# Kernel optimization log

Hardware: AMD Instinct MI355X
Metric: run time of the kernel (lower is better)

Reference implementation:

```python
import jax, jax.numpy as jnp
import numpy as np

N, E = 40000, 640000
D, H, DK = 128, 8, 16   # out_dim, n_heads, d_k = D // H
T, R = 3, 4             # num node types, num relation types


def setup_inputs() -> dict:
    key = jax.random.key(0)
    ks = jax.random.split(key, 16)
    glorot = lambda k, shape, fan: jax.random.normal(k, shape, jnp.float32) * np.sqrt(2.0 / fan)
    inp = {
        'node_inp': jax.random.normal(ks[0], (N, D), jnp.float32),
        'node_type': jax.random.randint(ks[1], (N,), 0, T),
        'edge_index': jax.random.randint(ks[2], (2, E), 0, N),
        'edge_type': jax.random.randint(ks[3], (E,), 0, R),
        'node_position': jax.random.randint(ks[4], (N,), 0, N),
        # per-node-type Linear weights, stored [T, in, out] (y = x @ W + b)
        'Kw': glorot(ks[5], (T, D, D), 2 * D), 'Kb': jnp.zeros((T, D), jnp.float32),
        'Qw': glorot(ks[6], (T, D, D), 2 * D), 'Qb': jnp.zeros((T, D), jnp.float32),
        'Vw': glorot(ks[7], (T, D, D), 2 * D), 'Vb': jnp.zeros((T, D), jnp.float32),
        'Aw': glorot(ks[8], (T, D, D), 2 * D), 'Ab': jnp.zeros((T, D), jnp.float32),
        'relation_pri': jnp.ones((T, R, T, H), jnp.float32),
        'relation_att': glorot(ks[9], (R, H, DK, DK), 2 * DK),
        'relation_msg': glorot(ks[10], (R, H, DK, DK), 2 * DK),
        'relation_s2u': glorot(ks[11], (D, D), 2 * D),
        'skip': jnp.ones((T,), jnp.float32),
    }
    return inp


def reference(node_inp, node_type, edge_index, edge_type, node_position,
              Kw, Kb, Qw, Qb, Vw, Vb, Aw, Ab,
              relation_pri, relation_att, relation_msg, relation_s2u, skip):
    n = node_inp.shape[0]
    src, tgt = edge_index[0], edge_index[1]  # j (source), i (target)
    ar = jnp.arange(n)

    # per-type K/Q/V projections for every node: [T, N, D], then select own type
    k_all = jnp.einsum('nd,tdo->tno', node_inp, Kw) + Kb[:, None, :]
    q_all = jnp.einsum('nd,tdo->tno', node_inp, Qw) + Qb[:, None, :]
    v_all = jnp.einsum('nd,tdo->tno', node_inp, Vw) + Vb[:, None, :]
    k_node = k_all[node_type, ar]
    q_node = q_all[node_type, ar]
    v_node = v_all[node_type, ar]

    k_j = k_node[src].reshape(-1, H, DK)
    v_j = v_node[src].reshape(-1, H, DK)
    q_i = q_node[tgt].reshape(-1, H, DK)

    # per-relation attention / message transforms (select per edge relation)
    k_t = jnp.zeros_like(k_j)
    v_t = jnp.zeros_like(v_j)
    for r in range(R):
        sel = (edge_type == r)[:, None, None]
        k_t = jnp.where(sel, jnp.einsum('ehd,hdf->ehf', k_j, relation_att[r]), k_t)
        v_t = jnp.where(sel, jnp.einsum('ehd,hdf->ehf', v_j, relation_msg[r]), v_t)

    st, tt = node_type[src], node_type[tgt]
    pri = relation_pri[tt, edge_type, st]                       # [E, H]
    att_raw = (q_i * k_t).sum(-1) * pri / np.sqrt(DK)           # [E, H]

    # scatter-softmax over edges sharing the same target node
    m = jax.ops.segment_max(att_raw, tgt, num_segments=n)
    m = jnp.where(jnp.isfinite(m), m, 0.0)
    ex = jnp.exp(att_raw - m[tgt])
    den = jax.ops.segment_sum(ex, tgt, num_segments=n)
    att = ex / (den[tgt] + 1e-16)

    msg = (v_t * att[:, :, None]).reshape(-1, D)
    aggr = jax.ops.segment_sum(msg, tgt, num_segments=n)        # scatter-add

    # speaker information: edges with edge_type==0, message from target rep to source index
    sp_in = v_all[1][tgt]                                       # v_linears[1](node_inp[edge_index_i])
    sp_msg = sp_in @ relation_s2u                               # [E, D]
    drop_idx = jnp.where(edge_type == 0, src, n)                # out-of-range -> dropped
    speaker_info = jnp.zeros((n, D), node_inp.dtype).at[drop_idx].set(sp_msg, mode='drop')

    aggr = jax.nn.gelu(aggr + speaker_info, approximate=False)

    # target-specific aggregation with per-type learnable skip (dropout=eval identity)
    a_all = jnp.einsum('no,tof->tnf', aggr, Aw) + Ab[:, None, :]
    a_node = a_all[node_type, ar]
    alpha = jax.nn.sigmoid(skip)[node_type][:, None]
    return a_node * alpha + node_inp * (1.0 - alpha)
```

## Files before the change

kernel.cpp:

```cpp
#include <hip/hip_runtime.h>
#include <hip/hip_bf16.h>
#include <math.h>

#define ND 128
#define NH 8
#define DKK 16
#define NT 3
#define NR 4
#define NB 8
#define NMAT 12
#define SCB 4096

typedef unsigned short ushort_t;
typedef __bf16 bf16_t;
typedef bf16_t bf16x8 __attribute__((ext_vector_type(8)));
typedef float f32x4 __attribute__((ext_vector_type(4)));

__device__ __forceinline__ float bf2f(unsigned short u) {
    union { unsigned int i; float f; } v; v.i = ((unsigned int)u) << 16; return v.f;
}
__device__ __forceinline__ unsigned short f2bf(float f) {
    union { float f; unsigned int i; } v; v.f = f;
    unsigned int x = v.i;
    unsigned int lsb = (x >> 16) & 1u;
    x += 0x7fffu + lsb;
    return (unsigned short)(x >> 16);
}
__device__ __forceinline__ unsigned int pk2(float a, float b) {
    return (unsigned int)f2bf(a) | ((unsigned int)f2bf(b) << 16);
}
__device__ __forceinline__ void load_bf8(const ushort_t* p, float* o) {
    uint4 u = *reinterpret_cast<const uint4*>(p);
    o[0]=bf2f(u.x & 0xffff); o[1]=bf2f(u.x >> 16);
    o[2]=bf2f(u.y & 0xffff); o[3]=bf2f(u.y >> 16);
    o[4]=bf2f(u.z & 0xffff); o[5]=bf2f(u.z >> 16);
    o[6]=bf2f(u.w & 0xffff); o[7]=bf2f(u.w >> 16);
}
__device__ __forceinline__ bf16x8 as_bf16x8(uint4 u) {
    union { uint4 u; bf16x8 v; } c; c.u = u; return c.v;
}


__global__ void k_zero(int n, int* offs, int* winner, int* tcnt) {
    int i = blockIdx.x * 256 + threadIdx.x;
    if (i < n) { offs[i] = 0; winner[i] = -1; }
    if (i < NT) tcnt[i] = 0;
}

__global__ void k_count(int n, int e, const int* src, const int* tgt, const int* etype,
                        const int* ntype, int* offs, int* winner, int* tcnt) {
    int i = blockIdx.x * 256 + threadIdx.x;
    if (i < e) {
        atomicAdd(&offs[tgt[i]], 1);
        if (etype[i] == 0) atomicMax(&winner[src[i]], i);
    }
    if (i < n) {
        int t = ntype[i];
        int lane = threadIdx.x & 63;
        #pragma unroll
        for (int tt = 0; tt < NT; tt++) {
            bool me = (t == tt);
            unsigned long long m = __ballot(me);
            if (me) {
                int lower = __popcll(m & ((1ull << lane) - 1ull));
                if (lower == 0) atomicAdd(&tcnt[tt], __popcll(m));
            }
        }
    }
}


__global__ void k_scanA(int n, const int* offs, int* bsum) {
    __shared__ int red[256];
    int b = blockIdx.x, tid = threadIdx.x;
    int base = b * SCB + tid * 16;
    int s = 0;
    #pragma unroll
    for (int i = 0; i < 16; i++) {
        int idx = base + i;
        if (idx < n) s += offs[idx];
    }
    red[tid] = s;
    __syncthreads();
    for (int d = 128; d > 0; d >>= 1) {
        if (tid < d) red[tid] += red[tid + d];
        __syncthreads();
    }
    if (tid == 0) bsum[b] = red[0];
}

__global__ void k_scanB(int nb, const int* bsum, int* boff,
                        const int* tcnt, int* tnext, int* tstart) {
    if (threadIdx.x == 0) {
        int run = 0;
        for (int b = 0; b < nb; b++) { boff[b] = run; run += bsum[b]; }
        int t0 = 0;
        for (int t = 0; t < NT; t++) { tnext[t] = t0; tstart[t] = t0; t0 += tcnt[t]; }
    }
}

__global__ void k_scanC(int n, int* offs, int* next, const int* boff) {
    __shared__ int red[256];
    int b = blockIdx.x, tid = threadIdx.x;
    int base = b * SCB + tid * 16;
    int v[16];
    int s = 0;
    #pragma unroll
    for (int i = 0; i < 16; i++) {
        int idx = base + i;
        v[i] = (idx < n) ? offs[idx] : 0;
        s += v[i];
    }
    red[tid] = s;
    __syncthreads();
    for (int d = 1; d < 256; d <<= 1) {
        int vv = (tid >= d) ? red[tid - d] : 0;
        __syncthreads();
        red[tid] += vv;
        __syncthreads();
    }
    int run = boff[b] + red[tid] - s;
    #pragma unroll
    for (int i = 0; i < 16; i++) {
        int idx = base + i;
        if (idx < n) { offs[idx] = run; next[idx] = run; run += v[i]; }
    }
    if (base <= n && n < base + 16) offs[n] = run;
}

__global__ void k_scatter(int n, int e, const int* src, const int* tgt, const int* etype,
                          const int* ntype, int* next, int* eord, int mode,
                          int* tnext, int* order) {
    int i = blockIdx.x * 256 + threadIdx.x;
    if (i < e) {
        int p = atomicAdd(&next[tgt[i]], 1);
        if (mode) {
            int s = src[i];
            eord[p] = (s * NR + etype[i]) | (ntype[s] << 28);
        } else {
            eord[p] = i;
        }
    }
    if (i < n) {
        int t = ntype[i];
        int lane = threadIdx.x & 63;
        #pragma unroll
        for (int tt = 0; tt < NT; tt++) {
            bool me = (t == tt);
            unsigned long long m = __ballot(me);
            if (me) {
                int lower = __popcll(m & ((1ull << lane) - 1ull));
                int leader = __ffsll((long long)m) - 1;
                int base = 0;
                if (lane == leader) base = atomicAdd(&tnext[tt], __popcll(m));
                base = __shfl(base, leader, 64);
                order[base + lower] = i;
            }
        }
    }
}


__global__ void k_pack(const float* Qw, const float* Qb, const float* Kw, const float* Kb,
                       const float* Vw, const float* Vb, const float* Aw, const float* Ab,
                       const float* s2u, const float* r_att, const float* r_msg,
                       ushort_t* Wall, float* bcat) {
    int blk = blockIdx.x;
    int kb = blk & 3;
    int c = (blk >> 2) & 7;
    int tm = blk >> 5;
    int m = tm % NMAT, t = tm / NMAT;
    int lane = threadIdx.x;
    int nn = c * 16 + (lane & 15);
    int quad = lane >> 4;
    int k0 = kb * 32 + quad * 8;
    ushort_t* dst = Wall + (size_t)blk * 512 + lane * 8;

    if (m == 0 || m == 5 || m == 10 || m == 11) {
        const float* W; const float* B;
        if (m == 0)       { W = Qw + (size_t)t * ND * ND; B = Qb + t * ND; }
        else if (m == 5)  { W = Vw + (size_t)ND * ND;     B = Vb + ND; }
        else if (m == 10) { W = Aw + (size_t)t * ND * ND; B = Ab + t * ND; }
        else              { W = s2u;                      B = nullptr; }
        #pragma unroll
        for (int j = 0; j < 8; j++) dst[j] = f2bf(W[(size_t)(k0 + j) * ND + nn]);
        if (kb == 0 && quad == 0)
            bcat[(t * NMAT + m) * ND + nn] = B ? B[nn] : 0.f;
    } else {
        int r = (m <= 4) ? (m - 1) : (m - 6);
        const float* W0 = (m <= 4) ? Kw : Vw;
        const float* B0 = (m <= 4) ? Kb : Vb;
        const float* Wr = (m <= 4) ? r_att : r_msg;
        int h = c, f = lane & 15;
        float wcol[16];
        #pragma unroll
        for (int jj = 0; jj < 16; jj++)
            wcol[jj] = Wr[(((size_t)r * NH + h) * DKK + jj) * DKK + f];
        #pragma unroll
        for (int j = 0; j < 8; j++) {
            const float* row = W0 + ((size_t)t * ND + (k0 + j)) * ND + h * DKK;
            float s = 0.f;
            #pragma unroll
            for (int jj = 0; jj < 16; jj++) s += row[jj] * wcol[jj];
            dst[j] = f2bf(s);
        }
        if (kb == 0 && quad == 0) {
            const float* brow = B0 + t * ND + h * DKK;
            float sb = 0.f;
            #pragma unroll
            for (int jj = 0; jj < 16; jj++) sb += brow[jj] * wcol[jj];
            bcat[(t * NMAT + m) * ND + nn] = sb;
        }
    }
}

__global__ void __launch_bounds__(256) k_projm(
    int n, const float* x_in, const int* order,
    const int* tcnt, const int* tstart,
    const ushort_t* Wall, const float* bcat,
    int m0, int nm,
    ushort_t* out_qn, ushort_t* out_kt, ushort_t* out_v1, ushort_t* out_vt)
{
    __shared__ __align__(16) ushort_t xs[4096];
    __shared__ int nodes[32];
    int b = blockIdx.x;
    int nb0 = (tcnt[0] + 31) >> 5, nb1 = (tcnt[1] + 31) >> 5, nb2 = (tcnt[2] + 31) >> 5;
    int t, lb;
    if (b < nb0)                  { t = 0; lb = b; }
    else if (b < nb0 + nb1)       { t = 1; lb = b - nb0; }
    else if (b < nb0 + nb1 + nb2) { t = 2; lb = b - nb0 - nb1; }
    else return;
    int segoff = lb * 32;
    int cnt = min(32, tcnt[t] - segoff);
    int segbase = tstart[t] + segoff;
    int tid = threadIdx.x;
    if (tid < 32) nodes[tid] = (tid < cnt) ? order[segbase + tid] : -1;
    __syncthreads();
    {
        int row = tid >> 3;
        int d0 = (tid & 7) * 16;
        int rt = row >> 4, rl = row & 15;
        int kb = d0 >> 5, q0 = (d0 >> 3) & 3;
        uint4 c0, c1;
        if (row < cnt) {
            const float4* xp4 = (const float4*)(x_in + (size_t)nodes[row] * ND + d0);
            float4 a = xp4[0], b2 = xp4[1], c2 = xp4[2], d4 = xp4[3];
            c0.x = pk2(a.x, a.y);   c0.y = pk2(a.z, a.w);
            c0.z = pk2(b2.x, b2.y); c0.w = pk2(b2.z, b2.w);
            c1.x = pk2(c2.x, c2.y); c1.y = pk2(c2.z, c2.w);
            c1.z = pk2(d4.x, d4.y); c1.w = pk2(d4.z, d4.w);
        } else {
            c0.x = c0.y = c0.z = c0.w = 0u;
            c1 = c0;
        }
        *(uint4*)&xs[((rt * 4 + kb) * 64 + q0 * 16 + rl) * 8]       = c0;
        *(uint4*)&xs[((rt * 4 + kb) * 64 + (q0 + 1) * 16 + rl) * 8] = c1;
    }
    __syncthreads();

    int w = tid >> 6, lane = tid & 63;
    int rt = w & 1;
    bf16x8 afr[4];
    #pragma unroll
    for (int kb = 0; kb < 4; kb++)
        afr[kb] = as_bf16x8(*(const uint4*)&xs[((rt * 4 + kb) * 64 + lane) * 8]);
    int nct = nm * 8;
    for (int ct = (w >> 1); ct < nct; ct += 2) {
        int m = m0 + (ct >> 3), c = ct & 7;
        const uint4* bp = (const uint4*)(Wall + ((((size_t)t * NMAT + m) * 8 + c) * 4) * 512);
        f32x4 acc = {0.f, 0.f, 0.f, 0.f};
        #pragma unroll
        for (int kb = 0; kb < 4; kb++) {
            bf16x8 bfr = as_bf16x8(bp[kb * 64 + lane]);
            acc = __builtin_amdgcn_mfma_f32_16x16x32_bf16(afr[kb], bfr, acc, 0, 0, 0);
        }
        int col = c * 16 + (lane & 15);
        float bias = bcat[(t * NMAT + m) * ND + col];
        int rbase = rt * 16 + (lane >> 4) * 4;
        #pragma unroll
        for (int r = 0; r < 4; r++) {
            int grow = rbase + r;
            if (grow >= cnt) continue;
            int node = nodes[grow];
            ushort_t val = f2bf(acc[r] + bias);
            if (m == 0)       out_qn[(size_t)node * ND + col] = val;
            else if (m <= 4)  out_kt[((size_t)node * NR + (m - 1)) * ND + col] = val;
            else if (m == 5)  out_v1[(size_t)node * ND + col] = val;
            else              out_vt[((size_t)node * NR + (m - 6)) * ND + col] = val;
        }
    }
}

__global__ void __launch_bounds__(256) k_spkm(
    int n, const int* winner, const int* tgt, const ushort_t* v1b,
    const ushort_t* Wall, float* aggr)
{
    __shared__ __align__(16) ushort_t xs[4096];
    __shared__ int wsrc[32];
    int base = blockIdx.x * 32;
    int cnt = min(32, n - base);
    if (cnt <= 0) return;
    int tid = threadIdx.x;
    if (tid < 32) {
        int w = (tid < cnt) ? winner[base + tid] : -1;
        wsrc[tid] = (w >= 0) ? tgt[w] : -1;
    }
    __syncthreads();
    {
        int row = tid >> 3;
        int d0 = (tid & 7) * 16;
        int rt = row >> 4, rl = row & 15;
        int kb = d0 >> 5, q0 = (d0 >> 3) & 3;
        uint4 c0, c1;
        int s = (row < cnt) ? wsrc[row] : -1;
        if (s >= 0) {
            const uint4* vp = (const uint4*)(v1b + (size_t)s * ND + d0);
            c0 = vp[0]; c1 = vp[1];
        } else { c0.x = c0.y = c0.z = c0.w = 0u; c1 = c0; }
        *(uint4*)&xs[((rt * 4 + kb) * 64 + q0 * 16 + rl) * 8]       = c0;
        *(uint4*)&xs[((rt * 4 + kb) * 64 + (q0 + 1) * 16 + rl) * 8] = c1;
    }
    __syncthreads();

    int w = tid >> 6, lane = tid & 63;
    int rt = w & 1;
    bf16x8 afr[4];
    #pragma unroll
    for (int kb = 0; kb < 4; kb++)
        afr[kb] = as_bf16x8(*(const uint4*)&xs[((rt * 4 + kb) * 64 + lane) * 8]);
    for (int ct = (w >> 1); ct < 8; ct += 2) {
        const uint4* bp = (const uint4*)(Wall + (((size_t)11 * 8 + ct) * 4) * 512);
        f32x4 acc = {0.f, 0.f, 0.f, 0.f};
        #pragma unroll
        for (int kb = 0; kb < 4; kb++) {
            bf16x8 bfr = as_bf16x8(bp[kb * 64 + lane]);
            acc = __builtin_amdgcn_mfma_f32_16x16x32_bf16(afr[kb], bfr, acc, 0, 0, 0);
        }
        int col = ct * 16 + (lane & 15);
        int rbase = rt * 16 + (lane >> 4) * 4;
        #pragma unroll
        for (int r = 0; r < 4; r++) {
            int grow = rbase + r;
            if (grow >= cnt) continue;
            size_t idx = (size_t)(base + grow) * ND + col;
            float g = aggr[idx] + acc[r];
            g = 0.5f * g * (1.f + erff(g * 0.70710678118f));
            aggr[idx] = g;
        }
    }
}

__global__ void __launch_bounds__(256) k_finalm(
    int n, const float* x_in, const int* order, const int* tcnt, const int* tstart,
    const ushort_t* Wall, const float* bcat, const float* skip,
    const float* aggr, float* out)
{
    __shared__ __align__(16) ushort_t xs[4096];
    __shared__ int nodes[32];
    int b = blockIdx.x;
    int nb0 = (tcnt[0] + 31) >> 5, nb1 = (tcnt[1] + 31) >> 5, nb2 = (tcnt[2] + 31) >> 5;
    int t, lb;
    if (b < nb0)                  { t = 0; lb = b; }
    else if (b < nb0 + nb1)       { t = 1; lb = b - nb0; }
    else if (b < nb0 + nb1 + nb2) { t = 2; lb = b - nb0 - nb1; }
    else return;
    int segoff = lb * 32;
    int cnt = min(32, tcnt[t] - segoff);
    int segbase = tstart[t] + segoff;
    int tid = threadIdx.x;
    if (tid < 32) nodes[tid] = (tid < cnt) ? order[segbase + tid] : -1;
    __syncthreads();
    {
        int row = tid >> 3;
        int d0 = (tid & 7) * 16;
        int rt = row >> 4, rl = row & 15;
        int kb = d0 >> 5, q0 = (d0 >> 3) & 3;
        uint4 c0, c1;
        if (row < cnt) {
            const float4* xp4 = (const float4*)(aggr + (size_t)nodes[row] * ND + d0);
            float4 a = xp4[0], b2 = xp4[1], c2 = xp4[2], d4 = xp4[3];
            c0.x = pk2(a.x, a.y);   c0.y = pk2(a.z, a.w);
            c0.z = pk2(b2.x, b2.y); c0.w = pk2(b2.z, b2.w);
            c1.x = pk2(c2.x, c2.y); c1.y = pk2(c2.z, c2.w);
            c1.z = pk2(d4.x, d4.y); c1.w = pk2(d4.z, d4.w);
        } else {
            c0.x = c0.y = c0.z = c0.w = 0u;
            c1 = c0;
        }
        *(uint4*)&xs[((rt * 4 + kb) * 64 + q0 * 16 + rl) * 8]       = c0;
        *(uint4*)&xs[((rt * 4 + kb) * 64 + (q0 + 1) * 16 + rl) * 8] = c1;
    }
    __syncthreads();

    float alpha = 1.f / (1.f + expf(-skip[t]));
    int w = tid >> 6, lane = tid & 63;
    int rt = w & 1;
    bf16x8 afr[4];
    #pragma unroll
    for (int kb = 0; kb < 4; kb++)
        afr[kb] = as_bf16x8(*(const uint4*)&xs[((rt * 4 + kb) * 64 + lane) * 8]);
    for (int ct = (w >> 1); ct < 8; ct += 2) {
        const uint4* bp = (const uint4*)(Wall + ((((size_t)t * NMAT + 10) * 8 + ct) * 4) * 512);
        f32x4 acc = {0.f, 0.f, 0.f, 0.f};
        #pragma unroll
        for (int kb = 0; kb < 4; kb++) {
            bf16x8 bfr = as_bf16x8(bp[kb * 64 + lane]);
            acc = __builtin_amdgcn_mfma_f32_16x16x32_bf16(afr[kb], bfr, acc, 0, 0, 0);
        }
        int col = ct * 16 + (lane & 15);
        float bias = bcat[(t * NMAT + 10) * ND + col];
        int rbase = rt * 16 + (lane >> 4) * 4;
        #pragma unroll
        for (int r = 0; r < 4; r++) {
            int grow = rbase + r;
            if (grow >= cnt) continue;
            int node = nodes[grow];
            float xin = x_in[(size_t)node * ND + col];
            out[(size_t)node * ND + col] = (acc[r] + bias) * alpha + xin * (1.f - alpha);
        }
    }
}

__global__ void __launch_bounds__(256) k_attmd(
    int n, const int* off, const int* srp, const int* ntype,
    const ushort_t* qn, const ushort_t* kt, const float* r_pri,
    float* atts, ushort_t* mb, float* db)
{
    int wv = threadIdx.x >> 6, lane = threadIdx.x & 63;
    int i = blockIdx.x * 4 + wv;
    if (i >= n) return;
    int h = lane & 7, slot = lane >> 3;
    int tt = ntype[i];
    float qf[16];
    load_bf8(qn + (size_t)i * ND + h * DKK, qf);
    load_bf8(qn + (size_t)i * ND + h * DKK + 8, qf + 8);
    const float* prib = r_pri + (size_t)(tt * NR * NT) * NH + h;
    int d0 = off[i], d1 = off[i + 1];
    float m = -3.0e38f, den = 0.f;
    #pragma unroll 2
    for (int p0 = d0; p0 < d1; p0 += 8) {
        int p = p0 + slot;
        bool live = (p < d1);
        int sp = live ? srp[p] : 0;
        int sr = sp & 0x0fffffff;
        int st = ((unsigned int)sp) >> 28;
        int r = sr & (NR - 1);
        float kf[16];
        const ushort_t* kp = kt + (size_t)sr * ND + h * DKK;
        load_bf8(kp, kf);
        load_bf8(kp + 8, kf + 8);
        float a = 0.f;
        #pragma unroll
        for (int f = 0; f < 16; f++) a += qf[f] * kf[f];
        float pri = prib[(r * NT + st) * NH];
        float logit = fminf(fmaxf(a * pri * 0.25f, -1.0e4f), 1.0e4f);
        if (live) {
            atts[(size_t)p * NH + h] = logit;
            float mnew = fmaxf(m, logit);
            den = den * expf(m - mnew) + expf(logit - mnew);
            m = mnew;
        }
    }
    #pragma unroll
    for (int d = 8; d < 64; d <<= 1) {
        float mo = __shfl_xor(m, d, 64);
        float dn = __shfl_xor(den, d, 64);
        float mnew = fmaxf(m, mo);
        den = den * expf(m - mnew) + dn * expf(mo - mnew);
        m = mnew;
    }
    if (slot == 0) {
        ushort_t mh = (d1 > d0) ? f2bf(m) : (ushort_t)0;
        float dfin = (d1 > d0) ? den * expf(m - bf2f(mh)) : 0.f;
        mb[i * NH + h] = mh;
        db[i * NH + h] = dfin;
    }
}

__global__ void __launch_bounds__(256) k_aggr_fast(
    int n, const int* off, const int* srp, const ushort_t* vt, const float* atts,
    const ushort_t* mb, const float* db, float* aggr)
{
    int wv = threadIdx.x >> 6, lane = threadIdx.x & 63;
    int i = blockIdx.x * 4 + wv;
    if (i >= n) return;
    int h = lane >> 3;
    float mref = bf2f(mb[i * NH + h]);
    float inv = 1.f / (db[i * NH + h] + 1e-16f);
    int d0 = off[i], d1 = off[i + 1];
    float acc0 = 0.f, acc1 = 0.f;
    #pragma unroll 4
    for (int p = d0; p < d1; p++) {
        int sr = srp[p] & 0x0fffffff;
        float w = expf(atts[(size_t)p * NH + h] - mref) * inv;
        unsigned int u = *reinterpret_cast<const unsigned int*>(
            vt + (size_t)sr * ND + lane * 2);
        acc0 += w * bf2f(u & 0xffff);
        acc1 += w * bf2f(u >> 16);
    }
    float2 o; o.x = acc0; o.y = acc1;
    *reinterpret_cast<float2*>(aggr + (size_t)i * ND + lane * 2) = o;
}


__global__ void k_proj(int n, const float* x_in, const int* ntype, const int* order,
                       const float* Kw, const float* Kb,
                       const float* Qw, const float* Qb,
                       const float* Vw, const float* Vb,
                       ushort_t* kn, ushort_t* qn, ushort_t* vn, ushort_t* v1) {
    __shared__ float xs[NB][ND];
    __shared__ int nodes[NB];
    __shared__ int types[NB];
    int tid = threadIdx.x;
    int base = blockIdx.x * NB;
    int cnt = min(NB, n - base);
    if (tid < cnt) { int nd = order[base + tid]; nodes[tid] = nd; types[tid] = ntype[nd]; }
    __syncthreads();
    for (int j = 0; j < cnt; j++) xs[j][tid] = x_in[(size_t)nodes[j] * ND + tid];
    __syncthreads();
    bool uni = (types[0] == types[cnt - 1]);
    for (int m = 0; m < 4; m++) {
        const float *W, *B; ushort_t* out; int forced_t = -1;
        if (m == 0)      { W = Kw; B = Kb; out = kn; }
        else if (m == 1) { W = Qw; B = Qb; out = qn; }
        else if (m == 2) { W = Vw; B = Vb; out = vn; }
        else             { W = Vw; B = Vb; out = v1; forced_t = 1; }
        if (uni || forced_t >= 0) {
            int t = (forced_t >= 0) ? forced_t : types[0];
            float bias = B[t * ND + tid];
            float acc[NB];
            #pragma unroll
            for (int j = 0; j < NB; j++) acc[j] = bias;
            const float* Wp = W + (size_t)t * ND * ND + tid;
            for (int d = 0; d < ND; d++) {
                float w = Wp[(size_t)d * ND];
                #pragma unroll
                for (int j = 0; j < NB; j++) acc[j] += xs[j][d] * w;
            }
            for (int j = 0; j < cnt; j++) out[(size_t)nodes[j] * ND + tid] = f2bf(acc[j]);
        } else {
            for (int j = 0; j < cnt; j++) {
                int t = types[j];
                float acc = B[t * ND + tid];
                const float* Wp = W + (size_t)t * ND * ND + tid;
                for (int d = 0; d < ND; d++) acc += xs[j][d] * Wp[(size_t)d * ND];
                out[(size_t)nodes[j] * ND + tid] = f2bf(acc);
            }
        }
    }
}

__global__ void k_att(int e, const int* src, const int* tgt, const int* etype, const int* ntype,
                      const ushort_t* kn, const ushort_t* qn,
                      const float* r_att, const float* r_pri, float* att) {
    int id = blockIdx.x * 256 + threadIdx.x;
    if (id >= e * NH) return;
    int ee = id >> 3, h = id & 7;
    int s = src[ee], t = tgt[ee], r = etype[ee];
    float kf[16], qf[16];
    load_bf8(kn + (size_t)s * ND + h * DKK, kf);
    load_bf8(kn + (size_t)s * ND + h * DKK + 8, kf + 8);
    load_bf8(qn + (size_t)t * ND + h * DKK, qf);
    load_bf8(qn + (size_t)t * ND + h * DKK + 8, qf + 8);
    const float* W = r_att + (size_t)(r * NH + h) * DKK * DKK;
    float kt[16];
    #pragma unroll
    for (int f = 0; f < 16; f++) kt[f] = 0.f;
    #pragma unroll 4
    for (int d = 0; d < 16; d++) {
        float kd = kf[d];
        #pragma unroll
        for (int f = 0; f < 16; f++) kt[f] += kd * W[d * 16 + f];
    }
    float a = 0.f;
    #pragma unroll
    for (int f = 0; f < 16; f++) a += qf[f] * kt[f];
    int tt = ntype[t], st = ntype[s];
    float pri = r_pri[((tt * NR + r) * NT + st) * NH + h];
    float logit = a * pri * 0.25f;
    logit = fminf(fmaxf(logit, -1.0e4f), 1.0e4f);
    att[(size_t)ee * NH + h] = logit;
}

__global__ void k_mden(int n, const int* off, const int* sorted,
                       const float* att, ushort_t* mb, float* db) {
    int id = blockIdx.x * 256 + threadIdx.x;
    if (id >= n * NH) return;
    int i = id >> 3, h = id & 7;
    int d0 = off[i], d1 = off[i + 1];
    float m = -3.0e38f;
    for (int p = d0; p < d1; p++) m = fmaxf(m, att[(size_t)sorted[p] * NH + h]);
    ushort_t mh = (d1 > d0) ? f2bf(m) : (ushort_t)0;
    float mref = bf2f(mh);
    float den = 0.f;
    for (int p = d0; p < d1; p++) den += expf(att[(size_t)sorted[p] * NH + h] - mref);
    mb[id] = mh;
    db[id] = den;
}

__global__ void k_norm(int e, const int* tgt, const ushort_t* mb, const float* db, float* att) {
    int id = blockIdx.x * 256 + threadIdx.x;
    if (id >= e * NH) return;
    int ee = id >> 3, h = id & 7;
    int t = tgt[ee];
    float w = expf(att[id] - bf2f(mb[t * NH + h])) / (db[t * NH + h] + 1e-16f);
    att[id] = w;
}

__global__ void k_aggr(int n, const int* off, const int* sorted, const int* src, const int* etype,
                       const ushort_t* vn, const float* r_msg, const float* att, float* aggr) {
    int wv = threadIdx.x >> 6, lane = threadIdx.x & 63;
    int i = blockIdx.x * 4 + wv;
    if (i >= n) return;
    int h = lane >> 3, f0 = (lane & 7) * 2;
    int d0 = off[i], d1 = off[i + 1];
    float acc0 = 0.f, acc1 = 0.f;
    for (int p = d0; p < d1; p++) {
        int ee = sorted[p];
        int s = src[ee], r = etype[ee];
        float w = att[(size_t)ee * NH + h];
        float vj[16];
        load_bf8(vn + (size_t)s * ND + h * DKK, vj);
        load_bf8(vn + (size_t)s * ND + h * DKK + 8, vj + 8);
        const float* Wm = r_msg + (size_t)(r * NH + h) * DKK * DKK + f0;
        float a0 = 0.f, a1 = 0.f;
        #pragma unroll
        for (int d = 0; d < 16; d++) {
            a0 += vj[d] * Wm[d * 16];
            a1 += vj[d] * Wm[d * 16 + 1];
        }
        acc0 += w * a0; acc1 += w * a1;
    }
    aggr[(size_t)i * ND + h * DKK + f0]     = acc0;
    aggr[(size_t)i * ND + h * DKK + f0 + 1] = acc1;
}

__global__ void k_spk(int n, const int* winner, const int* tgt, const ushort_t* v1,
                      const float* s2u, float* aggr) {
    __shared__ float xs[NB][ND];
    __shared__ int wn[NB];
    int tid = threadIdx.x;
    int base = blockIdx.x * NB;
    int cnt = min(NB, n - base);
    if (tid < cnt) wn[tid] = winner[base + tid];
    __syncthreads();
    for (int j = 0; j < cnt; j++) {
        int w = wn[j];
        xs[j][tid] = (w >= 0) ? bf2f(v1[(size_t)tgt[w] * ND + tid]) : 0.f;
    }
    __syncthreads();
    float acc[NB];
    #pragma unroll
    for (int j = 0; j < NB; j++) acc[j] = 0.f;
    const float* Wp = s2u + tid;
    for (int d = 0; d < ND; d++) {
        float w = Wp[(size_t)d * ND];
        #pragma unroll
        for (int j = 0; j < NB; j++) acc[j] += xs[j][d] * w;
    }
    for (int j = 0; j < cnt; j++) {
        size_t idx = (size_t)(base + j) * ND + tid;
        float g = aggr[idx] + acc[j];
        g = 0.5f * g * (1.f + erff(g * 0.70710678118f));
        aggr[idx] = g;
    }
}

__global__ void k_final(int n, const float* x_in, const int* ntype, const int* order,
                        const float* Aw, const float* Ab, const float* skip,
                        const float* aggr, float* out) {
    __shared__ float xs[NB][ND];
    __shared__ int nodes[NB];
    __shared__ int types[NB];
    int tid = threadIdx.x;
    int base = blockIdx.x * NB;
    int cnt = min(NB, n - base);
    if (tid < cnt) { int nd = order[base + tid]; nodes[tid] = nd; types[tid] = ntype[nd]; }
    __syncthreads();
    for (int j = 0; j < cnt; j++) xs[j][tid] = aggr[(size_t)nodes[j] * ND + tid];
    __syncthreads();
    bool uni = (types[0] == types[cnt - 1]);
    if (uni) {
        int t = types[0];
        float bias = Ab[t * ND + tid];
        float acc[NB];
        #pragma unroll
        for (int j = 0; j < NB; j++) acc[j] = bias;
        const float* Wp = Aw + (size_t)t * ND * ND + tid;
        for (int d = 0; d < ND; d++) {
            float w = Wp[(size_t)d * ND];
            #pragma unroll
            for (int j = 0; j < NB; j++) acc[j] += xs[j][d] * w;
        }
        float alpha = 1.f / (1.f + expf(-skip[t]));
        for (int j = 0; j < cnt; j++) {
            float xin = x_in[(size_t)nodes[j] * ND + tid];
            out[(size_t)nodes[j] * ND + tid] = acc[j] * alpha + xin * (1.f - alpha);
        }
    } else {
        for (int j = 0; j < cnt; j++) {
            int t = types[j];
            float acc = Ab[t * ND + tid];
            const float* Wp = Aw + (size_t)t * ND * ND + tid;
            for (int d = 0; d < ND; d++) acc += xs[j][d] * Wp[(size_t)d * ND];
            float alpha = 1.f / (1.f + expf(-skip[t]));
            float xin = x_in[(size_t)nodes[j] * ND + tid];
            out[(size_t)nodes[j] * ND + tid] = acc * alpha + xin * (1.f - alpha);
        }
    }
}

extern "C" void kernel_launch(void* const* d_in, const int* in_sizes, int n_in,
                              void* d_out, int out_size, void* d_ws, size_t ws_size,
                              hipStream_t stream) {
    const float* node_inp = (const float*)d_in[0];
    const int* node_type  = (const int*)d_in[1];
    const int* edge_index = (const int*)d_in[2];
    const int* edge_type  = (const int*)d_in[3];
    const float* Kw = (const float*)d_in[5];
    const float* Kb = (const float*)d_in[6];
    const float* Qw = (const float*)d_in[7];
    const float* Qb = (const float*)d_in[8];
    const float* Vw = (const float*)d_in[9];
    const float* Vb = (const float*)d_in[10];
    const float* Aw = (const float*)d_in[11];
    const float* Ab = (const float*)d_in[12];
    const float* r_pri = (const float*)d_in[13];
    const float* r_att = (const float*)d_in[14];
    const float* r_msg = (const float*)d_in[15];
    const float* s2u   = (const float*)d_in[16];
    const float* skip  = (const float*)d_in[17];

    int n = in_sizes[1];
    int e = in_sizes[3];
    const int* srcp = edge_index;
    const int* tgtp = edge_index + e;

    char* wsp = (char*)d_ws;
    size_t woff = 0;
    auto alloc = [&](size_t b) { void* p = wsp + woff; woff += (b + 255) & ~(size_t)255; return p; };

    int* offs     = (int*)alloc((size_t)(n + 1) * 4);
    int* nxt      = (int*)alloc((size_t)n * 4);
    int* winner   = (int*)alloc((size_t)n * 4);
    int* order    = (int*)alloc((size_t)n * 4);
    int* tcnt     = (int*)alloc(16);
    int* tnext    = (int*)alloc(16);
    int* tstart   = (int*)alloc(16);
    int* bsum     = (int*)alloc(4096);
    int* boff     = (int*)alloc(4096);
    int* eord     = (int*)alloc((size_t)e * 4);
    ushort_t* mb  = (ushort_t*)alloc((size_t)n * NH * 2);
    float* db     = (float*)alloc((size_t)n * NH * 4);
    ushort_t* v1b = (ushort_t*)alloc((size_t)n * ND * 2);
    float* att    = (float*)alloc((size_t)e * NH * 4);
    size_t commonEnd = woff;

    ushort_t* Wall  = (ushort_t*)alloc((size_t)NT * NMAT * 8 * 4 * 512 * 2);
    float* bcat     = (float*)alloc((size_t)NT * NMAT * ND * 4);
    char* F         = (char*)alloc((size_t)n * 1536);
    size_t fastEnd = woff;

    int gn = (n + 255) / 256;
    int ge = (e + 255) / 256;
    int nbscan = n / SCB + 1;
    int fast = (ws_size >= fastEnd) ? 1 : 0;

    k_zero<<<gn, 256, 0, stream>>>(n, offs, winner, tcnt);
    k_count<<<ge, 256, 0, stream>>>(n, e, srcp, tgtp, edge_type, node_type, offs, winner, tcnt);
    k_scanA<<<nbscan, 256, 0, stream>>>(n, offs, bsum);
    k_scanB<<<1, 64, 0, stream>>>(nbscan, bsum, boff, tcnt, tnext, tstart);
    k_scanC<<<nbscan, 256, 0, stream>>>(n, offs, nxt, boff);
    k_scatter<<<ge, 256, 0, stream>>>(n, e, srcp, tgtp, edge_type, node_type, nxt,
                                      eord, fast, tnext, order);

    if (fast) {
        ushort_t* qn  = (ushort_t*)F;
        ushort_t* kt  = (ushort_t*)(F + (size_t)n * 256);
        ushort_t* vt  = (ushort_t*)F;
        float* aggr   = (float*)(F + (size_t)n * 1024);
        int gproj = (n + 31) / 32 + NT;

        k_pack<<<NT * NMAT * 8 * 4, 64, 0, stream>>>(Qw, Qb, Kw, Kb, Vw, Vb, Aw, Ab,
                                                     s2u, r_att, r_msg, Wall, bcat);
        k_projm<<<gproj, 256, 0, stream>>>(n, node_inp, order, tcnt, tstart, Wall, bcat,
                                           0, 6, qn, kt, v1b, (ushort_t*)nullptr);
        k_attmd<<<(n + 3) / 4, 256, 0, stream>>>(n, offs, eord, node_type,
                                                 qn, kt, r_pri, att, mb, db);
        k_projm<<<gproj, 256, 0, stream>>>(n, node_inp, order, tcnt, tstart, Wall, bcat,
                                           6, 4, (ushort_t*)nullptr, (ushort_t*)nullptr,
                                           (ushort_t*)nullptr, vt);
        k_aggr_fast<<<(n + 3) / 4, 256, 0, stream>>>(n, offs, eord, vt, att, mb, db, aggr);
        k_spkm<<<(n + 31) / 32, 256, 0, stream>>>(n, winner, tgtp, v1b, Wall, aggr);
        k_finalm<<<gproj, 256, 0, stream>>>(n, node_inp, order, tcnt, tstart, Wall, bcat,
                                            skip, aggr, (float*)d_out);
    } else {
        woff = commonEnd;
        ushort_t* vn  = (ushort_t*)alloc((size_t)n * ND * 2);
        char* regA    = (char*)alloc((size_t)n * ND * 2 * 2);
        ushort_t* kn  = (ushort_t*)regA;
        ushort_t* qn  = (ushort_t*)(regA + (size_t)n * ND * 2);
        float* aggr   = (float*)regA;

        k_proj<<<(n + NB - 1) / NB, 128, 0, stream>>>(n, node_inp, node_type, order,
                                                      Kw, Kb, Qw, Qb, Vw, Vb, kn, qn, vn, v1b);
        k_att<<<(e * NH + 255) / 256, 256, 0, stream>>>(e, srcp, tgtp, edge_type, node_type,
                                                        kn, qn, r_att, r_pri, att);
        k_mden<<<(n * NH + 255) / 256, 256, 0, stream>>>(n, offs, eord, att, mb, db);
        k_norm<<<(e * NH + 255) / 256, 256, 0, stream>>>(e, tgtp, mb, db, att);
        k_aggr<<<(n + 3) / 4, 256, 0, stream>>>(n, offs, eord, srcp, edge_type, vn, r_msg, att, aggr);
        k_spk<<<(n + NB - 1) / NB, 128, 0, stream>>>(n, winner, tgtp, v1b, s2u, aggr);
        k_final<<<(n + NB - 1) / NB, 128, 0, stream>>>(n, node_inp, node_type, order,
                                                       Aw, Ab, skip, aggr, (float*)d_out);
    }
}
```

Baseline: 370.9 us.

## Fuse speaker GEMM+GELU into final projection kernel and record CSR ranks at count time

The speaker-info matmul and GELU are merged into the final per-type projection kernel. The GELU result stays in shared memory, so the float aggregate is no longer written back to global memory and read again, and one launch goes away. Separately, the count kernel now keeps each edge's atomicAdd return value as its rank. The scatter step then computes positions from offsets plus rank instead of doing a second atomic pass, which also removes the next array. The rank buffer aliases the attention buffer, and the fused kernel uses more shared memory, which may lower occupancy.

```diff
diff --git a/kernel.cpp b/kernel.cpp
--- a/kernel.cpp
+++ b/kernel.cpp
@@ -48,10 +48,10 @@
 }
 
 __global__ void k_count(int n, int e, const int* src, const int* tgt, const int* etype,
-                        const int* ntype, int* offs, int* winner, int* tcnt) {
+                        const int* ntype, int* offs, int* winner, int* tcnt, int* rank) {
     int i = blockIdx.x * 256 + threadIdx.x;
     if (i < e) {
-        atomicAdd(&offs[tgt[i]], 1);
+        rank[i] = atomicAdd(&offs[tgt[i]], 1);
         if (etype[i] == 0) atomicMax(&winner[src[i]], i);
     }
     if (i < n) {
@@ -99,7 +99,7 @@
     }
 }
 
-__global__ void k_scanC(int n, int* offs, int* next, const int* boff) {
+__global__ void k_scanC(int n, int* offs, const int* boff) {
     __shared__ int red[256];
     int b = blockIdx.x, tid = threadIdx.x;
     int base = b * SCB + tid * 16;
@@ -123,17 +123,17 @@
     #pragma unroll
     for (int i = 0; i < 16; i++) {
         int idx = base + i;
-        if (idx < n) { offs[idx] = run; next[idx] = run; run += v[i]; }
+        if (idx < n) { offs[idx] = run; run += v[i]; }
     }
     if (base <= n && n < base + 16) offs[n] = run;
 }
 
 __global__ void k_scatter(int n, int e, const int* src, const int* tgt, const int* etype,
-                          const int* ntype, int* next, int* eord, int mode,
-                          int* tnext, int* order) {
+                          const int* ntype, const int* offs, const int* rank,
+                          int* eord, int mode, int* tnext, int* order) {
     int i = blockIdx.x * 256 + threadIdx.x;
     if (i < e) {
-        int p = atomicAdd(&next[tgt[i]], 1);
+        int p = offs[tgt[i]] + rank[i];
         if (mode) {
             int s = src[i];
             eord[p] = (s * NR + etype[i]) | (ntype[s] << 28);
@@ -291,19 +291,32 @@
     }
 }
 
-__global__ void __launch_bounds__(256) k_spkm(
-    int n, const int* winner, const int* tgt, const ushort_t* v1b,
-    const ushort_t* Wall, float* aggr)
+__global__ void __launch_bounds__(256) k_sfinal(
+    int n, const float* x_in, const int* order, const int* tcnt, const int* tstart,
+    const int* winner, const int* tgt, const ushort_t* v1b,
+    const ushort_t* Wall, const float* bcat, const float* skip,
+    const float* aggr, float* out)
 {
+    __shared__ __align__(16) float xf[32 * 132];
     __shared__ __align__(16) ushort_t xs[4096];
+    __shared__ int nodes[32];
     __shared__ int wsrc[32];
-    int base = blockIdx.x * 32;
-    int cnt = min(32, n - base);
-    if (cnt <= 0) return;
+    int b = blockIdx.x;
+    int nb0 = (tcnt[0] + 31) >> 5, nb1 = (tcnt[1] + 31) >> 5, nb2 = (tcnt[2] + 31) >> 5;
+    int t, lb;
+    if (b < nb0)                  { t = 0; lb = b; }
+    else if (b < nb0 + nb1)       { t = 1; lb = b - nb0; }
+    else if (b < nb0 + nb1 + nb2) { t = 2; lb = b - nb0 - nb1; }
+    else return;
+    int segoff = lb * 32;
+    int cnt = min(32, tcnt[t] - segoff);
+    int segbase = tstart[t] + segoff;
     int tid = threadIdx.x;
     if (tid < 32) {
-        int w = (tid < cnt) ? winner[base + tid] : -1;
-        wsrc[tid] = (w >= 0) ? tgt[w] : -1;
+        int nd = (tid < cnt) ? order[segbase + tid] : -1;
+        nodes[tid] = nd;
+        int wi = (nd >= 0) ? winner[nd] : -1;
+        wsrc[tid] = (wi >= 0) ? tgt[wi] : -1;
     }
     __syncthreads();
     {
@@ -321,63 +334,43 @@
         *(uint4*)&xs[((rt * 4 + kb) * 64 + (q0 + 1) * 16 + rl) * 8] = c1;
     }
     __syncthreads();
-
     int w = tid >> 6, lane = tid & 63;
     int rt = w & 1;
-    bf16x8 afr[4];
-    #pragma unroll
-    for (int kb = 0; kb < 4; kb++)
-        afr[kb] = as_bf16x8(*(const uint4*)&xs[((rt * 4 + kb) * 64 + lane) * 8]);
-    for (int ct = (w >> 1); ct < 8; ct += 2) {
-        const uint4* bp = (const uint4*)(Wall + (((size_t)11 * 8 + ct) * 4) * 512);
-        f32x4 acc = {0.f, 0.f, 0.f, 0.f};
-        #pragma unroll
-        for (int kb = 0; kb < 4; kb++) {
-            bf16x8 bfr = as_bf16x8(bp[kb * 64 + lane]);
-            acc = __builtin_amdgcn_mfma_f32_16x16x32_bf16(afr[kb], bfr, acc, 0, 0, 0);
-        }
-        int col = ct * 16 + (lane & 15);
-        int rbase = rt * 16 + (lane >> 4) * 4;
-        #pragma unroll
-        for (int r = 0; r < 4; r++) {
-            int grow = rbase + r;
-            if (grow >= cnt) continue;
-            size_t idx = (size_t)(base + grow) * ND + col;
-            float g = aggr[idx] + acc[r];
-            g = 0.5f * g * (1.f + erff(g * 0.70710678118f));
-            aggr[idx] = g;
-        }
-    }
-}
-
-__global__ void __launch_bounds__(256) k_finalm(
-    int n, const float* x_in, const int* order, const int* tcnt, const int* tstart,
-    const ushort_t* Wall, const float* bcat, const float* skip,
-    const float* aggr, float* out)
-{
-    __shared__ __align__(16) ushort_t xs[4096];
-    __shared__ int nodes[32];
-    int b = blockIdx.x;
-    int nb0 = (tcnt[0] + 31) >> 5, nb1 = (tcnt[1] + 31) >> 5, nb2 = (tcnt[2] + 31) >> 5;
-    int t, lb;
-    if (b < nb0)                  { t = 0; lb = b; }
-    else if (b < nb0 + nb1)       { t = 1; lb = b - nb0; }
-    else if (b < nb0 + nb1 + nb2) { t = 2; lb = b - nb0 - nb1; }
-    else return;
-    int segoff = lb * 32;
-    int cnt = min(32, tcnt[t] - segoff);
-    int segbase = tstart[t] + segoff;
-    int tid = threadIdx.x;
-    if (tid < 32) nodes[tid] = (tid < cnt) ? order[segbase + tid] : -1;
+    {
+        bf16x8 afr[4];
+        #pragma unroll
+        for (int kb = 0; kb < 4; kb++)
+            afr[kb] = as_bf16x8(*(const uint4*)&xs[((rt * 4 + kb) * 64 + lane) * 8]);
+        for (int ct = (w >> 1); ct < 8; ct += 2) {
+            const uint4* bp = (const uint4*)(Wall + (((size_t)11 * 8 + ct) * 4) * 512);
+            f32x4 acc = {0.f, 0.f, 0.f, 0.f};
+            #pragma unroll
+            for (int kb = 0; kb < 4; kb++) {
+                bf16x8 bfr = as_bf16x8(bp[kb * 64 + lane]);
+                acc = __builtin_amdgcn_mfma_f32_16x16x32_bf16(afr[kb], bfr, acc, 0, 0, 0);
+            }
+            int col = ct * 16 + (lane & 15);
+            int rbase = rt * 16 + (lane >> 4) * 4;
+            #pragma unroll
+            for (int r = 0; r < 4; r++) {
+                int grow = rbase + r;
+                if (grow >= cnt) continue;
+                int node = nodes[grow];
+                float g = aggr[(size_t)node * ND + col] + acc[r];
+                g = 0.5f * g * (1.f + erff(g * 0.70710678118f));
+                xf[grow * 132 + col] = g;
+            }
+        }
+    }
     __syncthreads();
     {
         int row = tid >> 3;
         int d0 = (tid & 7) * 16;
-        int rt = row >> 4, rl = row & 15;
+        int rt2 = row >> 4, rl = row & 15;
         int kb = d0 >> 5, q0 = (d0 >> 3) & 3;
         uint4 c0, c1;
         if (row < cnt) {
-            const float4* xp4 = (const float4*)(aggr + (size_t)nodes[row] * ND + d0);
+            const float4* xp4 = (const float4*)(xf + row * 132 + d0);
             float4 a = xp4[0], b2 = xp4[1], c2 = xp4[2], d4 = xp4[3];
             c0.x = pk2(a.x, a.y);   c0.y = pk2(a.z, a.w);
             c0.z = pk2(b2.x, b2.y); c0.w = pk2(b2.z, b2.w);
@@ -387,36 +380,35 @@
             c0.x = c0.y = c0.z = c0.w = 0u;
             c1 = c0;
         }
-        *(uint4*)&xs[((rt * 4 + kb) * 64 + q0 * 16 + rl) * 8]       = c0;
-        *(uint4*)&xs[((rt * 4 + kb) * 64 + (q0 + 1) * 16 + rl) * 8] = c1;
-    }
-    __syncthreads();
-
+        *(uint4*)&xs[((rt2 * 4 + kb) * 64 + q0 * 16 + rl) * 8]       = c0;
+        *(uint4*)&xs[((rt2 * 4 + kb) * 64 + (q0 + 1) * 16 + rl) * 8] = c1;
+    }
+    __syncthreads();
     float alpha = 1.f / (1.f + expf(-skip[t]));
-    int w = tid >> 6, lane = tid & 63;
-    int rt = w & 1;
-    bf16x8 afr[4];
-    #pragma unroll
-    for (int kb = 0; kb < 4; kb++)
-        afr[kb] = as_bf16x8(*(const uint4*)&xs[((rt * 4 + kb) * 64 + lane) * 8]);
-    for (int ct = (w >> 1); ct < 8; ct += 2) {
-        const uint4* bp = (const uint4*)(Wall + ((((size_t)t * NMAT + 10) * 8 + ct) * 4) * 512);
-        f32x4 acc = {0.f, 0.f, 0.f, 0.f};
-        #pragma unroll
-        for (int kb = 0; kb < 4; kb++) {
-            bf16x8 bfr = as_bf16x8(bp[kb * 64 + lane]);
-            acc = __builtin_amdgcn_mfma_f32_16x16x32_bf16(afr[kb], bfr, acc, 0, 0, 0);
-        }
-        int col = ct * 16 + (lane & 15);
-        float bias = bcat[(t * NMAT + 10) * ND + col];
-        int rbase = rt * 16 + (lane >> 4) * 4;
-        #pragma unroll
-        for (int r = 0; r < 4; r++) {
-            int grow = rbase + r;
-            if (grow >= cnt) continue;
-            int node = nodes[grow];
-            float xin = x_in[(size_t)node * ND + col];
-            out[(size_t)node * ND + col] = (acc[r] + bias) * alpha + xin * (1.f - alpha);
+    {
+        bf16x8 afr[4];
+        #pragma unroll
+        for (int kb = 0; kb < 4; kb++)
+            afr[kb] = as_bf16x8(*(const uint4*)&xs[((rt * 4 + kb) * 64 + lane) * 8]);
+        for (int ct = (w >> 1); ct < 8; ct += 2) {
+            const uint4* bp = (const uint4*)(Wall + ((((size_t)t * NMAT + 10) * 8 + ct) * 4) * 512);
+            f32x4 acc = {0.f, 0.f, 0.f, 0.f};
+            #pragma unroll
+            for (int kb = 0; kb < 4; kb++) {
+                bf16x8 bfr = as_bf16x8(bp[kb * 64 + lane]);
+                acc = __builtin_amdgcn_mfma_f32_16x16x32_bf16(afr[kb], bfr, acc, 0, 0, 0);
+            }
+            int col = ct * 16 + (lane & 15);
+            float bias = bcat[(t * NMAT + 10) * ND + col];
+            int rbase = rt * 16 + (lane >> 4) * 4;
+            #pragma unroll
+            for (int r = 0; r < 4; r++) {
+                int grow = rbase + r;
+                if (grow >= cnt) continue;
+                int node = nodes[grow];
+                float xin = x_in[(size_t)node * ND + col];
+                out[(size_t)node * ND + col] = (acc[r] + bias) * alpha + xin * (1.f - alpha);
+            }
         }
     }
 }
@@ -741,7 +733,6 @@
     auto alloc = [&](size_t b) { void* p = wsp + woff; woff += (b + 255) & ~(size_t)255; return p; };
 
     int* offs     = (int*)alloc((size_t)(n + 1) * 4);
-    int* nxt      = (int*)alloc((size_t)n * 4);
     int* winner   = (int*)alloc((size_t)n * 4);
     int* order    = (int*)alloc((size_t)n * 4);
     int* tcnt     = (int*)alloc(16);
@@ -756,6 +747,8 @@
     float* att    = (float*)alloc((size_t)e * NH * 4);
     size_t commonEnd = woff;
 
+    int* rank = (int*)att;
+
     ushort_t* Wall  = (ushort_t*)alloc((size_t)NT * NMAT * 8 * 4 * 512 * 2);
     float* bcat     = (float*)alloc((size_t)NT * NMAT * ND * 4);
     char* F         = (char*)alloc((size_t)n * 1536);
@@ -767,11 +760,11 @@
     int fast = (ws_size >= fastEnd) ? 1 : 0;
 
     k_zero<<<gn, 256, 0, stream>>>(n, offs, winner, tcnt);
-    k_count<<<ge, 256, 0, stream>>>(n, e, srcp, tgtp, edge_type, node_type, offs, winner, tcnt);
+    k_count<<<ge, 256, 0, stream>>>(n, e, srcp, tgtp, edge_type, node_type, offs, winner, tcnt, rank);
     k_scanA<<<nbscan, 256, 0, stream>>>(n, offs, bsum);
     k_scanB<<<1, 64, 0, stream>>>(nbscan, bsum, boff, tcnt, tnext, tstart);
-    k_scanC<<<nbscan, 256, 0, stream>>>(n, offs, nxt, boff);
-    k_scatter<<<ge, 256, 0, stream>>>(n, e, srcp, tgtp, edge_type, node_type, nxt,
+    k_scanC<<<nbscan, 256, 0, stream>>>(n, offs, boff);
+    k_scatter<<<ge, 256, 0, stream>>>(n, e, srcp, tgtp, edge_type, node_type, offs, rank,
                                       eord, fast, tnext, order);
 
     if (fast) {
@@ -791,9 +784,9 @@
                                            6, 4, (ushort_t*)nullptr, (ushort_t*)nullptr,
                                            (ushort_t*)nullptr, vt);
         k_aggr_fast<<<(n + 3) / 4, 256, 0, stream>>>(n, offs, eord, vt, att, mb, db, aggr);
-        k_spkm<<<(n + 31) / 32, 256, 0, stream>>>(n, winner, tgtp, v1b, Wall, aggr);
-        k_finalm<<<gproj, 256, 0, stream>>>(n, node_inp, order, tcnt, tstart, Wall, bcat,
-                                            skip, aggr, (float*)d_out);
+        k_sfinal<<<gproj, 256, 0, stream>>>(n, node_inp, order, tcnt, tstart,
+                                            winner, tgtp, v1b, Wall, bcat, skip,
+                                            aggr, (float*)d_out);
     } else {
         woff = commonEnd;
         ushort_t* vn  = (ushort_t*)alloc((size_t)n * ND * 2);
```

New measurement: 352.9 us. -4.8%, faster.
